# Kernel tuning notes

Hardware: AMD Instinct MI355X
Metric: run time of the kernel (lower is better)

Reference implementation:

```python
import jax, jax.numpy as jnp
import numpy as np

OUT_SIZE, EMB, DEC_H, ENC_D = 172, 128, 256, 256
B, L = 256, 1024


def setup_inputs() -> dict:
    key = jax.random.key(0)
    ks = jax.random.split(key, 16)
    s = lambda k, shp, scale=0.05: (jax.random.normal(k, shp, dtype=jnp.float32) * scale)
    return {
        "h0": jax.random.normal(ks[0], (B, DEC_H), dtype=jnp.float32),
        "c0": jax.random.normal(ks[1], (B, DEC_H), dtype=jnp.float32),
        "o_t": jax.random.normal(ks[2], (B, DEC_H), dtype=jnp.float32),
        "enc_out": jax.random.normal(ks[3], (B, L, ENC_D), dtype=jnp.float32),
        "lasttarget": jax.random.randint(ks[4], (B, 1), 0, OUT_SIZE),
        # learned params
        "emb": s(ks[5], (OUT_SIZE, EMB), 1.0),
        "W_ih": s(ks[6], (4 * DEC_H, DEC_H + EMB)),
        "W_hh": s(ks[7], (4 * DEC_H, DEC_H)),
        "b_ih": s(ks[8], (4 * DEC_H,)),
        "b_hh": s(ks[9], (4 * DEC_H,)),
        "W1": s(ks[10], (ENC_D, ENC_D)),
        "W2": s(ks[11], (ENC_D, DEC_H)),
        "W3": s(ks[12], (DEC_H, DEC_H + ENC_D)),
        "W_out": s(ks[13], (OUT_SIZE, DEC_H)),
        "beta": jax.random.uniform(ks[14], (ENC_D,), dtype=jnp.float32, minval=-0.01, maxval=0.01),
    }


def reference(h0, c0, o_t, enc_out, lasttarget, emb, W_ih, W_hh, b_ih, b_hh, W1, W2, W3, W_out, beta):
    # embedding + concat -> LSTMCell input (B, DEC_H+EMB)
    prev_y = emb[lasttarget[:, 0]]              # (B, EMB)
    inp = jnp.concatenate([prev_y, o_t], axis=1)
    # LSTMCell: gate order i, f, g, o (PyTorch convention)
    gates = inp @ W_ih.T + b_ih + h0 @ W_hh.T + b_hh   # (B, 4*DEC_H)
    i, f, g, o = jnp.split(gates, 4, axis=1)
    c_t = jax.nn.sigmoid(f) * c0 + jax.nn.sigmoid(i) * jnp.tanh(g)
    h_t = jax.nn.sigmoid(o) * jnp.tanh(c_t)
    # additive attention over enc positions
    alpha = jnp.tanh(enc_out @ W1.T + (h_t @ W2.T)[:, None, :])  # (B, L, ENC_D)
    scores = jnp.sum(beta * alpha, axis=-1)                      # (B, L)
    attn = jax.nn.softmax(scores, axis=-1)
    context = jnp.einsum("bl,bld->bd", attn, enc_out)            # (B, ENC_D)
    # output projection
    o_new = jnp.tanh(jnp.concatenate([h_t, context], axis=1) @ W3.T)  # (B, DEC_H)
    logit = jax.nn.softmax(o_new @ W_out.T, axis=1)                   # (B, OUT_SIZE)
    return (h_t, c_t, o_new, logit)
```

## Files before the change

### kernel.cpp

```cpp
#include <hip/hip_runtime.h>

#define B_   256
#define L_   1024
#define H_   256
#define EMB_ 128
#define OUT_ 172

typedef float f32x4 __attribute__((ext_vector_type(4)));
typedef __bf16 bf16x8 __attribute__((ext_vector_type(8)));
typedef unsigned short us8 __attribute__((ext_vector_type(8)));

static __device__ __forceinline__ unsigned short f2bf(float f) {
    __bf16 h = (__bf16)f;
    return __builtin_bit_cast(unsigned short, h);
}
static __device__ __forceinline__ us8 pack8(float4 x0, float4 x1) {
    bf16x8 v;
    v[0]=(__bf16)x0.x; v[1]=(__bf16)x0.y; v[2]=(__bf16)x0.z; v[3]=(__bf16)x0.w;
    v[4]=(__bf16)x1.x; v[5]=(__bf16)x1.y; v[6]=(__bf16)x1.z; v[7]=(__bf16)x1.w;
    return __builtin_bit_cast(us8, v);
}
static __device__ __forceinline__ us8 cvt8(const float* __restrict__ p) {
    return pack8(*(const float4*)p, *(const float4*)(p + 4));
}
static __device__ __forceinline__ float tanh_fast(float x) {
    float e = __expf(2.f * x);
    return 1.f - 2.f * __builtin_amdgcn_rcpf(e + 1.f);
}
static __device__ __forceinline__ float sigm_fast(float x) {
    return __builtin_amdgcn_rcpf(1.f + __expf(-x));
}

static __device__ __forceinline__ void barrier_lgkm() {
    __builtin_amdgcn_sched_barrier(0);
    asm volatile("s_waitcnt lgkmcnt(0)" ::: "memory");
    __builtin_amdgcn_s_barrier();
    __builtin_amdgcn_sched_barrier(0);
}

#define TS  40
#define TS2 72

__global__ __launch_bounds__(256) void k_gates(
    const float* __restrict__ h0, const float* __restrict__ o_t,
    const int* __restrict__ lasttarget, const float* __restrict__ emb,
    const float* __restrict__ W_ih, const float* __restrict__ W_hh,
    const float* __restrict__ b_ih, const float* __restrict__ b_hh,
    float* __restrict__ gates)
{
    const int m0 = (blockIdx.x >> 4) * 64;
    const int n0 = (blockIdx.x & 15) * 64;
    const int tid = threadIdx.x;
    const int w = tid >> 6, lane = tid & 63, quad = lane >> 4, l15 = lane & 15;

    __shared__ __align__(16) unsigned short As[2][64 * TS2];
    __shared__ __align__(16) unsigned short Bs[2][64 * TS2];

    float bias[4];
    #pragma unroll
    for (int nt = 0; nt < 4; nt++) {
        int n = n0 + nt * 16 + l15;
        bias[nt] = b_ih[n] + b_hh[n];
    }

    f32x4 acc[4] = {{0,0,0,0},{0,0,0,0},{0,0,0,0},{0,0,0,0}};
    const int sm = tid >> 2, sk8 = (tid & 3) * 8;
    const int row = m0 + sm;
    const int lt = lasttarget[row];
    const int j  = n0 + sm;

    float4 xa0, xa1, xa2, xa3, xb0, xb1, xb2, xb3;
    {
        const float* a0 = emb + lt * EMB_ + sk8;
        const float* a1 = a0 + 32;
        xa0 = *(const float4*)a0; xa1 = *(const float4*)(a0 + 4);
        xa2 = *(const float4*)a1; xa3 = *(const float4*)(a1 + 4);
        const float* b0 = W_ih + j * 384 + sk8;
        const float* b1 = b0 + 32;
        xb0 = *(const float4*)b0; xb1 = *(const float4*)(b0 + 4);
        xb2 = *(const float4*)b1; xb3 = *(const float4*)(b1 + 4);
    }

    for (int kc = 0; kc < 10; kc++) {
        const int buf = kc & 1;
        *(us8*)&As[buf][sm * TS2 + sk8]      = pack8(xa0, xa1);
        *(us8*)&As[buf][sm * TS2 + 32 + sk8] = pack8(xa2, xa3);
        *(us8*)&Bs[buf][sm * TS2 + sk8]      = pack8(xb0, xb1);
        *(us8*)&Bs[buf][sm * TS2 + 32 + sk8] = pack8(xb2, xb3);
        if (kc < 9) {
            const int k0 = (kc + 1) * 64 + sk8;
            const int k1 = k0 + 32;
            const float* a0 = (k0 < 128) ? emb + lt * EMB_ + k0
                            : (k0 < 384) ? o_t + row * H_ + (k0 - 128)
                                         : h0  + row * H_ + (k0 - 384);
            const float* a1 = (k1 < 128) ? emb + lt * EMB_ + k1
                            : (k1 < 384) ? o_t + row * H_ + (k1 - 128)
                                         : h0  + row * H_ + (k1 - 384);
            xa0 = *(const float4*)a0; xa1 = *(const float4*)(a0 + 4);
            xa2 = *(const float4*)a1; xa3 = *(const float4*)(a1 + 4);
            const float* b0 = (k0 < 384) ? W_ih + j * 384 + k0 : W_hh + j * 256 + (k0 - 384);
            const float* b1 = (k1 < 384) ? W_ih + j * 384 + k1 : W_hh + j * 256 + (k1 - 384);
            xb0 = *(const float4*)b0; xb1 = *(const float4*)(b0 + 4);
            xb2 = *(const float4*)b1; xb3 = *(const float4*)(b1 + 4);
        }
        barrier_lgkm();
        #pragma unroll
        for (int c = 0; c < 2; c++) {
            bf16x8 a = __builtin_bit_cast(bf16x8, *(const us8*)&As[buf][(w * 16 + l15) * TS2 + c * 32 + quad * 8]);
            #pragma unroll
            for (int nt = 0; nt < 4; nt++) {
                bf16x8 b = __builtin_bit_cast(bf16x8, *(const us8*)&Bs[buf][(nt * 16 + l15) * TS2 + c * 32 + quad * 8]);
                acc[nt] = __builtin_amdgcn_mfma_f32_16x16x32_bf16(a, b, acc[nt], 0, 0, 0);
            }
        }
    }
    #pragma unroll
    for (int nt = 0; nt < 4; nt++)
        #pragma unroll
        for (int r = 0; r < 4; r++)
            gates[(m0 + w * 16 + quad * 4 + r) * 1024 + n0 + nt * 16 + l15] = acc[nt][r] + bias[nt];
}

__global__ __launch_bounds__(256) void k_lstm(
    const float* __restrict__ gates, const float* __restrict__ c0,
    const float* __restrict__ W2,
    float* __restrict__ out, unsigned short* __restrict__ A3u,
    float* __restrict__ hW2)
{
    const int b = blockIdx.x, t = threadIdx.x;
    const float* g = gates + b * 1024;
    float gi = g[t], gf = g[256 + t], gg = g[512 + t], go = g[768 + t];
    float c = sigm_fast(gf) * c0[b * H_ + t] + sigm_fast(gi) * tanh_fast(gg);
    float h = sigm_fast(go) * tanh_fast(c);
    out[b * H_ + t]           = h;
    out[B_ * H_ + b * H_ + t] = c;
    A3u[b * 256 + t] = f2bf(h);

    __shared__ float hs[256];
    hs[t] = h;
    barrier_lgkm();
    float acc = 0.f;
    const float* w2r = W2 + t * 256;
    #pragma unroll 4
    for (int k = 0; k < 256; k += 8) {
        float4 wa = *(const float4*)(w2r + k);
        float4 wb = *(const float4*)(w2r + k + 4);
        acc += hs[k]*wa.x + hs[k+1]*wa.y + hs[k+2]*wa.z + hs[k+3]*wa.w
             + hs[k+4]*wb.x + hs[k+5]*wb.y + hs[k+6]*wb.z + hs[k+7]*wb.w;
    }
    hW2[b * 256 + t] = acc;
}

#define ROWSTR 264

__global__ __launch_bounds__(512, 2) void k_attn(
    const float* __restrict__ enc, const float* __restrict__ W1,
    const float* __restrict__ hW2, const float* __restrict__ beta,
    float* __restrict__ ctx_part, float* __restrict__ s_part)
{
    const int blk = blockIdx.x;
    const int b = blk >> 1, half = blk & 1;
    const int tid = threadIdx.x;
    const int wave = tid >> 6, lane = tid & 63;
    const int quad = lane >> 4, l15 = lane & 15;

    __shared__ __align__(16) unsigned short encs[4][16 * ROWSTR];
    __shared__ float sp[2][8][16];
    __shared__ float wexp[2][16];
    __shared__ float2 cr[512];

    bf16x8 wf[8][2];
    float hw2v[2], betav[2];
    #pragma unroll
    for (int nt = 0; nt < 2; nt++) {
        int n = wave * 32 + nt * 16 + l15;
        hw2v[nt]  = hW2[b * H_ + n];
        betav[nt] = beta[n];
        #pragma unroll
        for (int ks = 0; ks < 8; ks++)
            wf[ks][nt] = __builtin_bit_cast(bf16x8, cvt8(W1 + n * 256 + ks * 32 + quad * 8));
    }

    const float* encb = enc + ((size_t)b * L_ + half * 512) * H_;
    const int srow = tid >> 5, scol = (tid & 31) * 8;

    *(us8*)&encs[0][srow * ROWSTR + scol] = cvt8(encb + srow * 256 + scol);
    float4 x0, x1;
    {
        const float* p = encb + 16 * 256 + srow * 256 + scol;
        x0 = *(const float4*)p; x1 = *(const float4*)(p + 4);
    }
    barrier_lgkm();

    const int cp = tid & 127, q = tid >> 7;
    float2 ctx2 = {0.f, 0.f};
    float ssum = 0.f;

    for (int it = 0; it < 34; it++) {
        float4 y0 = {0,0,0,0}, y1 = {0,0,0,0};
        if (it < 30) {
            const float* p = encb + (size_t)(it + 2) * 16 * 256 + srow * 256 + scol;
            y0 = *(const float4*)p; y1 = *(const float4*)(p + 4);
        }
        if (it >= 1 && it <= 32 && tid < 16) {
            const int pp = (it - 1) & 1;
            float sc = sp[pp][0][tid] + sp[pp][1][tid] + sp[pp][2][tid] + sp[pp][3][tid]
                     + sp[pp][4][tid] + sp[pp][5][tid] + sp[pp][6][tid] + sp[pp][7][tid];
            wexp[pp][tid] = __expf(sc);
        }
        if (it >= 2) {
            const int pb = (it - 2) & 3, pp = (it - 2) & 1;
            const unsigned* base = (const unsigned*)&encs[pb][0];
            float cx = ctx2.x, cy = ctx2.y;
            #pragma unroll
            for (int r = 0; r < 4; r++) {
                const int row = q * 4 + r;
                unsigned u = base[row * (ROWSTR / 2) + cp];
                float wv = wexp[pp][row];
                cx += wv * __uint_as_float(u << 16);
                cy += wv * __uint_as_float(u & 0xffff0000u);
            }
            ctx2.x = cx; ctx2.y = cy;
            if (tid == 0) {
                float s2 = 0.f;
                #pragma unroll
                for (int r = 0; r < 16; r++) s2 += wexp[pp][r];
                ssum += s2;
            }
        }
        if (it < 32) {
            f32x4 acc0 = {0,0,0,0}, acc1 = {0,0,0,0};
            const unsigned short* arow = &encs[it & 3][l15 * ROWSTR + quad * 8];
            #pragma unroll
            for (int ks = 0; ks < 8; ks++) {
                bf16x8 a = __builtin_bit_cast(bf16x8, *(const us8*)(arow + ks * 32));
                acc0 = __builtin_amdgcn_mfma_f32_16x16x32_bf16(a, wf[ks][0], acc0, 0, 0, 0);
                acc1 = __builtin_amdgcn_mfma_f32_16x16x32_bf16(a, wf[ks][1], acc1, 0, 0, 0);
            }
            float p4[4];
            #pragma unroll
            for (int r = 0; r < 4; r++) {
                float t0 = tanh_fast(acc0[r] + hw2v[0]);
                float t1 = tanh_fast(acc1[r] + hw2v[1]);
                p4[r] = betav[0] * t0 + betav[1] * t1;
            }
            #pragma unroll
            for (int m = 1; m < 16; m <<= 1) {
                p4[0] += __shfl_xor(p4[0], m);
                p4[1] += __shfl_xor(p4[1], m);
                p4[2] += __shfl_xor(p4[2], m);
                p4[3] += __shfl_xor(p4[3], m);
            }
            if (l15 == 0) {
                #pragma unroll
                for (int r = 0; r < 4; r++) sp[it & 1][wave][quad * 4 + r] = p4[r];
            }
        }
        if (it < 31)
            *(us8*)&encs[(it + 1) & 3][srow * ROWSTR + scol] = pack8(x0, x1);
        barrier_lgkm();
        x0 = y0; x1 = y1;
    }
    cr[tid] = ctx2;
    barrier_lgkm();
    if (tid == 0) s_part[blk] = ssum;
    if (tid < 128) {
        float2 a0 = cr[tid], a1 = cr[tid + 128], a2 = cr[tid + 256], a3 = cr[tid + 384];
        float2 o;
        o.x = a0.x + a1.x + a2.x + a3.x;
        o.y = a0.y + a1.y + a2.y + a3.y;
        ((float2*)ctx_part)[blk * 128 + tid] = o;
    }
}

__global__ __launch_bounds__(256) void k_out3(
    const unsigned short* __restrict__ A3u, const float* __restrict__ ctx_part,
    const float* __restrict__ s_part, const float* __restrict__ W3,
    float* __restrict__ out, unsigned short* __restrict__ A4u)
{
    const int m0 = (blockIdx.x >> 2) * 64;
    const int n0 = (blockIdx.x & 3) * 64;
    const int tid = threadIdx.x;
    const int w = tid >> 6, lane = tid & 63, quad = lane >> 4, l15 = lane & 15;
    __shared__ __align__(16) unsigned short As[2][64 * TS];
    __shared__ __align__(16) unsigned short Bs[2][64 * TS];
    f32x4 acc[4] = {{0,0,0,0},{0,0,0,0},{0,0,0,0},{0,0,0,0}};
    const int sm = tid >> 2, sk8 = (tid & 3) * 8;
    const int bb = m0 + sm;
    const float inv = 1.f / (s_part[2 * bb] + s_part[2 * bb + 1]);

    us8 au = *(const us8*)&A3u[bb * 256 + sk8];
    float4 ca0, ca1, cb0, cb1;
    float4 wb0, wb1;
    { const float* bp = W3 + (n0 + sm) * 512 + sk8;
      wb0 = *(const float4*)bp; wb1 = *(const float4*)(bp + 4); }

    for (int kc = 0; kc < 16; kc++) {
        const int buf = kc & 1;
        if (kc < 8) {
            *(us8*)&As[buf][sm * TS + sk8] = au;
        } else {
            bf16x8 v;
            v[0]=(__bf16)((ca0.x+cb0.x)*inv); v[1]=(__bf16)((ca0.y+cb0.y)*inv);
            v[2]=(__bf16)((ca0.z+cb0.z)*inv); v[3]=(__bf16)((ca0.w+cb0.w)*inv);
            v[4]=(__bf16)((ca1.x+cb1.x)*inv); v[5]=(__bf16)((ca1.y+cb1.y)*inv);
            v[6]=(__bf16)((ca1.z+cb1.z)*inv); v[7]=(__bf16)((ca1.w+cb1.w)*inv);
            *(us8*)&As[buf][sm * TS + sk8] = __builtin_bit_cast(us8, v);
        }
        *(us8*)&Bs[buf][sm * TS + sk8] = pack8(wb0, wb1);
        if (kc < 15) {
            const int k = (kc + 1) * 32 + sk8;
            if (kc + 1 < 8) {
                au = *(const us8*)&A3u[bb * 256 + k];
            } else {
                const int c = k - 256;
                const float* p0 = ctx_part + (size_t)(2 * bb) * 256 + c;
                const float* p1 = ctx_part + (size_t)(2 * bb + 1) * 256 + c;
                ca0 = *(const float4*)p0; ca1 = *(const float4*)(p0 + 4);
                cb0 = *(const float4*)p1; cb1 = *(const float4*)(p1 + 4);
            }
            const float* bp = W3 + (n0 + sm) * 512 + k;
            wb0 = *(const float4*)bp; wb1 = *(const float4*)(bp + 4);
        }
        barrier_lgkm();
        bf16x8 a = __builtin_bit_cast(bf16x8, *(const us8*)&As[buf][(w * 16 + l15) * TS + quad * 8]);
        #pragma unroll
        for (int nt = 0; nt < 4; nt++) {
            bf16x8 b = __builtin_bit_cast(bf16x8, *(const us8*)&Bs[buf][(nt * 16 + l15) * TS + quad * 8]);
            acc[nt] = __builtin_amdgcn_mfma_f32_16x16x32_bf16(a, b, acc[nt], 0, 0, 0);
        }
    }
    #pragma unroll
    for (int nt = 0; nt < 4; nt++)
        #pragma unroll
        for (int r = 0; r < 4; r++) {
            int row = m0 + w * 16 + quad * 4 + r, col = n0 + nt * 16 + l15;
            float o = tanh_fast(acc[nt][r]);
            out[2 * B_ * H_ + row * 256 + col] = o;
            A4u[row * 256 + col] = f2bf(o);
        }
}

__global__ __launch_bounds__(256) void k_logit(
    const unsigned short* __restrict__ A4u, const float* __restrict__ W_out,
    float* __restrict__ out)
{
    const int m0 = blockIdx.x * 32;
    const int tid = threadIdx.x;
    const int w = tid >> 6, lane = tid & 63, quad = lane >> 4, l15 = lane & 15;
    const int r2 = w >> 1, ch = w & 1;
    __shared__ __align__(16) unsigned short As[2][32 * TS];
    __shared__ __align__(16) unsigned short Bs[2][192 * TS];
    __shared__ float lg[32][196];
    f32x4 acc[6];
    #pragma unroll
    for (int nt = 0; nt < 6; nt++) acc[nt] = (f32x4){0,0,0,0};
    const int sm = tid >> 2, sk8 = (tid & 3) * 8;
    const int j0 = sm, j1 = 64 + sm, j2 = 128 + sm;

    us8 au = {0,0,0,0,0,0,0,0};
    if (tid < 128) au = *(const us8*)&A4u[(m0 + sm) * 256 + sk8];
    float4 w0a, w0b, w1a, w1b, w2a = {0,0,0,0}, w2b = {0,0,0,0};
    { const float* p = W_out + j0 * 256 + sk8; w0a = *(const float4*)p; w0b = *(const float4*)(p + 4); }
    { const float* p = W_out + j1 * 256 + sk8; w1a = *(const float4*)p; w1b = *(const float4*)(p + 4); }
    if (j2 < OUT_) { const float* p = W_out + j2 * 256 + sk8; w2a = *(const float4*)p; w2b = *(const float4*)(p + 4); }

    for (int kc = 0; kc < 8; kc++) {
        const int buf = kc & 1;
        if (tid < 128) *(us8*)&As[buf][sm * TS + sk8] = au;
        *(us8*)&Bs[buf][j0 * TS + sk8] = pack8(w0a, w0b);
        *(us8*)&Bs[buf][j1 * TS + sk8] = pack8(w1a, w1b);
        *(us8*)&Bs[buf][j2 * TS + sk8] = pack8(w2a, w2b);
        if (kc < 7) {
            const int k = (kc + 1) * 32 + sk8;
            if (tid < 128) au = *(const us8*)&A4u[(m0 + sm) * 256 + k];
            { const float* p = W_out + j0 * 256 + k; w0a = *(const float4*)p; w0b = *(const float4*)(p + 4); }
            { const float* p = W_out + j1 * 256 + k; w1a = *(const float4*)p; w1b = *(const float4*)(p + 4); }
            if (j2 < OUT_) { const float* p = W_out + j2 * 256 + k; w2a = *(const float4*)p; w2b = *(const float4*)(p + 4); }
        }
        barrier_lgkm();
        bf16x8 a = __builtin_bit_cast(bf16x8, *(const us8*)&As[buf][(r2 * 16 + l15) * TS + quad * 8]);
        #pragma unroll
        for (int nt = 0; nt < 6; nt++) {
            bf16x8 b = __builtin_bit_cast(bf16x8, *(const us8*)&Bs[buf][(ch * 96 + nt * 16 + l15) * TS + quad * 8]);
            acc[nt] = __builtin_amdgcn_mfma_f32_16x16x32_bf16(a, b, acc[nt], 0, 0, 0);
        }
    }
    #pragma unroll
    for (int nt = 0; nt < 6; nt++)
        #pragma unroll
        for (int r = 0; r < 4; r++)
            lg[r2 * 16 + quad * 4 + r][ch * 96 + nt * 16 + l15] = acc[nt][r];
    __syncthreads();
    const int m = tid >> 2, p = tid & 3;
    if (m < 32) {
        const int cb = p * 43;
        float mx = -1e30f;
        for (int c = 0; c < 43; c++) mx = fmaxf(mx, lg[m][cb + c]);
        mx = fmaxf(mx, __shfl_xor(mx, 1));
        mx = fmaxf(mx, __shfl_xor(mx, 2));
        float s = 0.f;
        for (int c = 0; c < 43; c++) { float e = __expf(lg[m][cb + c] - mx); lg[m][cb + c] = e; s += e; }
        s += __shfl_xor(s, 1);
        s += __shfl_xor(s, 2);
        float inv = 1.f / s;
        for (int c = 0; c < 43; c++)
            out[3 * B_ * H_ + (m0 + m) * OUT_ + cb + c] = lg[m][cb + c] * inv;
    }
}

extern "C" void kernel_launch(void* const* d_in, const int* in_sizes, int n_in,
                              void* d_out, int out_size, void* d_ws, size_t ws_size,
                              hipStream_t stream)
{
    const float* h0   = (const float*)d_in[0];
    const float* c0   = (const float*)d_in[1];
    const float* o_t  = (const float*)d_in[2];
    const float* enc  = (const float*)d_in[3];
    const int*   lt   = (const int*)  d_in[4];
    const float* emb  = (const float*)d_in[5];
    const float* W_ih = (const float*)d_in[6];
    const float* W_hh = (const float*)d_in[7];
    const float* b_ih = (const float*)d_in[8];
    const float* b_hh = (const float*)d_in[9];
    const float* W1   = (const float*)d_in[10];
    const float* W2   = (const float*)d_in[11];
    const float* W3   = (const float*)d_in[12];
    const float* Wo   = (const float*)d_in[13];
    const float* beta = (const float*)d_in[14];
    float* out = (float*)d_out;
    float* ws  = (float*)d_ws;

    float*          gates    = ws;
    float*          hW2      = ws + 262144;
    float*          ctx_part = ws + 327680;
    float*          s_part   = ws + 458752;
    unsigned short* A3u      = (unsigned short*)(ws + 459264);
    unsigned short* A4u      = (unsigned short*)(ws + 492032);

    k_gates<<<64, 256, 0, stream>>>(h0, o_t, lt, emb, W_ih, W_hh, b_ih, b_hh, gates);
    k_lstm <<<256, 256, 0, stream>>>(gates, c0, W2, out, A3u, hW2);
    k_attn <<<512, 512, 0, stream>>>(enc, W1, hW2, beta, ctx_part, s_part);
    k_out3 <<<16, 256, 0, stream>>>(A3u, ctx_part, s_part, W3, out, A4u);
    k_logit<<<8, 256, 0, stream>>>(A4u, Wo, out);
}
```

Baseline: 437.2 us.

## Fuse LSTM gate GEMM with cell update and fold h·W2 into attention

The gates GEMM now computes all four gate blocks for a 64-column slice in each workgroup, so the LSTM cell nonlinearity runs in the epilogue and the gates buffer round-trip disappears. The h_t·W2ᵀ matvec moves from the separate LSTM kernel into the start of each attention block, which reads h_t from the output buffer. This removes one launch and the intermediate global writes. The cost is a gates kernel of only 16 workgroups, which leaves most CUs idle, and the W2 matvec is now recomputed redundantly by both attention halves of each batch row.

```diff
diff --git a/kernel.cpp b/kernel.cpp
--- a/kernel.cpp
+++ b/kernel.cpp
@@ -38,124 +38,102 @@
     __builtin_amdgcn_sched_barrier(0);
 }
 
-#define TS  40
-#define TS2 72
-
-__global__ __launch_bounds__(256) void k_gates(
+#define TS 40
+
+__global__ __launch_bounds__(256) void k_gateslstm(
     const float* __restrict__ h0, const float* __restrict__ o_t,
     const int* __restrict__ lasttarget, const float* __restrict__ emb,
     const float* __restrict__ W_ih, const float* __restrict__ W_hh,
     const float* __restrict__ b_ih, const float* __restrict__ b_hh,
-    float* __restrict__ gates)
+    const float* __restrict__ c0,
+    float* __restrict__ out, unsigned short* __restrict__ A3u)
 {
-    const int m0 = (blockIdx.x >> 4) * 64;
-    const int n0 = (blockIdx.x & 15) * 64;
+    const int m0  = (blockIdx.x >> 2) * 64;
+    const int c0c = (blockIdx.x & 3) * 64;
     const int tid = threadIdx.x;
     const int w = tid >> 6, lane = tid & 63, quad = lane >> 4, l15 = lane & 15;
 
-    __shared__ __align__(16) unsigned short As[2][64 * TS2];
-    __shared__ __align__(16) unsigned short Bs[2][64 * TS2];
-
-    float bias[4];
-    #pragma unroll
-    for (int nt = 0; nt < 4; nt++) {
-        int n = n0 + nt * 16 + l15;
+    __shared__ __align__(16) unsigned short As[2][64 * TS];
+    __shared__ __align__(16) unsigned short Bs[2][256 * TS];
+
+    float bias[16];
+    #pragma unroll
+    for (int nt = 0; nt < 16; nt++) {
+        int n = (nt >> 2) * 256 + c0c + (nt & 3) * 16 + l15;
         bias[nt] = b_ih[n] + b_hh[n];
     }
 
-    f32x4 acc[4] = {{0,0,0,0},{0,0,0,0},{0,0,0,0},{0,0,0,0}};
+    f32x4 acc[16];
+    #pragma unroll
+    for (int nt = 0; nt < 16; nt++) acc[nt] = (f32x4){0,0,0,0};
+
     const int sm = tid >> 2, sk8 = (tid & 3) * 8;
-    const int row = m0 + sm;
-    const int lt = lasttarget[row];
-    const int j  = n0 + sm;
-
-    float4 xa0, xa1, xa2, xa3, xb0, xb1, xb2, xb3;
+    const int arow = m0 + sm;
+    const int lt = lasttarget[arow];
+    const int jj = tid;
+    const int wrow = (jj >> 6) * 256 + c0c + (jj & 63);
+
+    float4 xa0, xa1, xb[8];
     {
-        const float* a0 = emb + lt * EMB_ + sk8;
-        const float* a1 = a0 + 32;
-        xa0 = *(const float4*)a0; xa1 = *(const float4*)(a0 + 4);
-        xa2 = *(const float4*)a1; xa3 = *(const float4*)(a1 + 4);
-        const float* b0 = W_ih + j * 384 + sk8;
-        const float* b1 = b0 + 32;
-        xb0 = *(const float4*)b0; xb1 = *(const float4*)(b0 + 4);
-        xb2 = *(const float4*)b1; xb3 = *(const float4*)(b1 + 4);
-    }
-
-    for (int kc = 0; kc < 10; kc++) {
+        const float* ap = emb + lt * EMB_ + sk8;
+        xa0 = *(const float4*)ap; xa1 = *(const float4*)(ap + 4);
+        const float* bp = W_ih + wrow * 384;
+        #pragma unroll
+        for (int i = 0; i < 8; i++) xb[i] = *(const float4*)(bp + i * 4);
+    }
+
+    for (int kc = 0; kc < 20; kc++) {
         const int buf = kc & 1;
-        *(us8*)&As[buf][sm * TS2 + sk8]      = pack8(xa0, xa1);
-        *(us8*)&As[buf][sm * TS2 + 32 + sk8] = pack8(xa2, xa3);
-        *(us8*)&Bs[buf][sm * TS2 + sk8]      = pack8(xb0, xb1);
-        *(us8*)&Bs[buf][sm * TS2 + 32 + sk8] = pack8(xb2, xb3);
-        if (kc < 9) {
-            const int k0 = (kc + 1) * 64 + sk8;
-            const int k1 = k0 + 32;
-            const float* a0 = (k0 < 128) ? emb + lt * EMB_ + k0
-                            : (k0 < 384) ? o_t + row * H_ + (k0 - 128)
-                                         : h0  + row * H_ + (k0 - 384);
-            const float* a1 = (k1 < 128) ? emb + lt * EMB_ + k1
-                            : (k1 < 384) ? o_t + row * H_ + (k1 - 128)
-                                         : h0  + row * H_ + (k1 - 384);
-            xa0 = *(const float4*)a0; xa1 = *(const float4*)(a0 + 4);
-            xa2 = *(const float4*)a1; xa3 = *(const float4*)(a1 + 4);
-            const float* b0 = (k0 < 384) ? W_ih + j * 384 + k0 : W_hh + j * 256 + (k0 - 384);
-            const float* b1 = (k1 < 384) ? W_ih + j * 384 + k1 : W_hh + j * 256 + (k1 - 384);
-            xb0 = *(const float4*)b0; xb1 = *(const float4*)(b0 + 4);
-            xb2 = *(const float4*)b1; xb3 = *(const float4*)(b1 + 4);
+        *(us8*)&As[buf][sm * TS + sk8] = pack8(xa0, xa1);
+        #pragma unroll
+        for (int i = 0; i < 4; i++)
+            *(us8*)&Bs[buf][jj * TS + i * 8] = pack8(xb[2 * i], xb[2 * i + 1]);
+        if (kc < 19) {
+            const int k = (kc + 1) * 32 + sk8;
+            const float* ap = (k < 128) ? emb + lt * EMB_ + k
+                            : (k < 384) ? o_t + arow * H_ + (k - 128)
+                                        : h0  + arow * H_ + (k - 384);
+            xa0 = *(const float4*)ap; xa1 = *(const float4*)(ap + 4);
+            const int kb = (kc + 1) * 32;
+            const float* bp = (kb < 384) ? W_ih + wrow * 384 + kb
+                                         : W_hh + wrow * 256 + (kb - 384);
+            #pragma unroll
+            for (int i = 0; i < 8; i++) xb[i] = *(const float4*)(bp + i * 4);
         }
         barrier_lgkm();
-        #pragma unroll
-        for (int c = 0; c < 2; c++) {
-            bf16x8 a = __builtin_bit_cast(bf16x8, *(const us8*)&As[buf][(w * 16 + l15) * TS2 + c * 32 + quad * 8]);
-            #pragma unroll
-            for (int nt = 0; nt < 4; nt++) {
-                bf16x8 b = __builtin_bit_cast(bf16x8, *(const us8*)&Bs[buf][(nt * 16 + l15) * TS2 + c * 32 + quad * 8]);
-                acc[nt] = __builtin_amdgcn_mfma_f32_16x16x32_bf16(a, b, acc[nt], 0, 0, 0);
-            }
-        }
-    }
-    #pragma unroll
-    for (int nt = 0; nt < 4; nt++)
-        #pragma unroll
-        for (int r = 0; r < 4; r++)
-            gates[(m0 + w * 16 + quad * 4 + r) * 1024 + n0 + nt * 16 + l15] = acc[nt][r] + bias[nt];
-}
-
-__global__ __launch_bounds__(256) void k_lstm(
-    const float* __restrict__ gates, const float* __restrict__ c0,
-    const float* __restrict__ W2,
-    float* __restrict__ out, unsigned short* __restrict__ A3u,
-    float* __restrict__ hW2)
-{
-    const int b = blockIdx.x, t = threadIdx.x;
-    const float* g = gates + b * 1024;
-    float gi = g[t], gf = g[256 + t], gg = g[512 + t], go = g[768 + t];
-    float c = sigm_fast(gf) * c0[b * H_ + t] + sigm_fast(gi) * tanh_fast(gg);
-    float h = sigm_fast(go) * tanh_fast(c);
-    out[b * H_ + t]           = h;
-    out[B_ * H_ + b * H_ + t] = c;
-    A3u[b * 256 + t] = f2bf(h);
-
-    __shared__ float hs[256];
-    hs[t] = h;
-    barrier_lgkm();
-    float acc = 0.f;
-    const float* w2r = W2 + t * 256;
-    #pragma unroll 4
-    for (int k = 0; k < 256; k += 8) {
-        float4 wa = *(const float4*)(w2r + k);
-        float4 wb = *(const float4*)(w2r + k + 4);
-        acc += hs[k]*wa.x + hs[k+1]*wa.y + hs[k+2]*wa.z + hs[k+3]*wa.w
-             + hs[k+4]*wb.x + hs[k+5]*wb.y + hs[k+6]*wb.z + hs[k+7]*wb.w;
-    }
-    hW2[b * 256 + t] = acc;
+        bf16x8 a = __builtin_bit_cast(bf16x8, *(const us8*)&As[buf][(w * 16 + l15) * TS + quad * 8]);
+        #pragma unroll
+        for (int nt = 0; nt < 16; nt++) {
+            bf16x8 b = __builtin_bit_cast(bf16x8, *(const us8*)&Bs[buf][(nt * 16 + l15) * TS + quad * 8]);
+            acc[nt] = __builtin_amdgcn_mfma_f32_16x16x32_bf16(a, b, acc[nt], 0, 0, 0);
+        }
+    }
+
+    #pragma unroll
+    for (int ncc = 0; ncc < 4; ncc++) {
+        #pragma unroll
+        for (int r = 0; r < 4; r++) {
+            const int row = m0 + w * 16 + quad * 4 + r;
+            const int col = c0c + ncc * 16 + l15;
+            float gi = acc[0 * 4 + ncc][r] + bias[0 * 4 + ncc];
+            float gf = acc[1 * 4 + ncc][r] + bias[1 * 4 + ncc];
+            float gg = acc[2 * 4 + ncc][r] + bias[2 * 4 + ncc];
+            float go = acc[3 * 4 + ncc][r] + bias[3 * 4 + ncc];
+            float c = sigm_fast(gf) * c0[row * H_ + col] + sigm_fast(gi) * tanh_fast(gg);
+            float h = sigm_fast(go) * tanh_fast(c);
+            out[row * H_ + col]           = h;
+            out[B_ * H_ + row * H_ + col] = c;
+            A3u[row * 256 + col] = f2bf(h);
+        }
+    }
 }
 
 #define ROWSTR 264
 
 __global__ __launch_bounds__(512, 2) void k_attn(
     const float* __restrict__ enc, const float* __restrict__ W1,
-    const float* __restrict__ hW2, const float* __restrict__ beta,
+    const float* __restrict__ hvec, const float* __restrict__ W2,
+    const float* __restrict__ beta,
     float* __restrict__ ctx_part, float* __restrict__ s_part)
 {
     const int blk = blockIdx.x;
@@ -168,13 +146,33 @@
     __shared__ float sp[2][8][16];
     __shared__ float wexp[2][16];
     __shared__ float2 cr[512];
+    __shared__ float hs[256];
+    __shared__ float hw2p[512];
+
+    if (tid < 256) hs[tid] = hvec[b * H_ + tid];
+    barrier_lgkm();
+    {
+        const int dn = tid >> 1, hf = tid & 1;
+        const float* w2r = W2 + dn * 256 + hf * 128;
+        const float* hsr = hs + hf * 128;
+        float a = 0.f;
+        #pragma unroll 4
+        for (int k = 0; k < 128; k += 8) {
+            float4 wa = *(const float4*)(w2r + k);
+            float4 wb = *(const float4*)(w2r + k + 4);
+            a += hsr[k]*wa.x + hsr[k+1]*wa.y + hsr[k+2]*wa.z + hsr[k+3]*wa.w
+               + hsr[k+4]*wb.x + hsr[k+5]*wb.y + hsr[k+6]*wb.z + hsr[k+7]*wb.w;
+        }
+        hw2p[tid] = a;
+    }
+    barrier_lgkm();
 
     bf16x8 wf[8][2];
     float hw2v[2], betav[2];
     #pragma unroll
     for (int nt = 0; nt < 2; nt++) {
         int n = wave * 32 + nt * 16 + l15;
-        hw2v[nt]  = hW2[b * H_ + n];
+        hw2v[nt]  = hw2p[2 * n] + hw2p[2 * n + 1];
         betav[nt] = beta[n];
         #pragma unroll
         for (int ks = 0; ks < 8; ks++)
@@ -431,16 +429,13 @@
     float* out = (float*)d_out;
     float* ws  = (float*)d_ws;
 
-    float*          gates    = ws;
-    float*          hW2      = ws + 262144;
     float*          ctx_part = ws + 327680;
     float*          s_part   = ws + 458752;
     unsigned short* A3u      = (unsigned short*)(ws + 459264);
     unsigned short* A4u      = (unsigned short*)(ws + 492032);
 
-    k_gates<<<64, 256, 0, stream>>>(h0, o_t, lt, emb, W_ih, W_hh, b_ih, b_hh, gates);
-    k_lstm <<<256, 256, 0, stream>>>(gates, c0, W2, out, A3u, hW2);
-    k_attn <<<512, 512, 0, stream>>>(enc, W1, hW2, beta, ctx_part, s_part);
+    k_gateslstm<<<16, 256, 0, stream>>>(h0, o_t, lt, emb, W_ih, W_hh, b_ih, b_hh, c0, out, A3u);
+    k_attn <<<512, 512, 0, stream>>>(enc, W1, out , W2, beta, ctx_part, s_part);
     k_out3 <<<16, 256, 0, stream>>>(A3u, ctx_part, s_part, W3, out, A4u);
     k_logit<<<8, 256, 0, stream>>>(A4u, Wo, out);
 }
```

Result: slower. 458.9 us (+5.0%).
